# Performance work log

Hardware: AMD Instinct MI355X
Metric: run time of the kernel (lower is better)

## Reference

```python
import jax, jax.numpy as jnp
import numpy as np

N_NODES = 100000
N_EDGES = 600000
IN_SIZE = 128
OUT_SIZE = 128
N_GRAPHS = 100
BN_EPS = 1e-5


def setup_inputs() -> dict:
    key = jax.random.key(0)
    ks = jax.random.split(key, 8)
    h = jax.random.normal(ks[0], (N_NODES, IN_SIZE), dtype=jnp.float32)
    norm = jax.random.uniform(ks[1], (N_NODES, 1), dtype=jnp.float32)
    src = jax.random.randint(ks[2], (N_EDGES,), 0, N_NODES, dtype=jnp.int32)
    dst = jax.random.randint(ks[3], (N_EDGES,), 0, N_NODES, dtype=jnp.int32)
    graph_ids = jnp.sort(jax.random.randint(ks[4], (N_NODES,), 0, N_GRAPHS, dtype=jnp.int32))
    # Linear + BatchNorm params
    W = jax.random.normal(ks[5], (IN_SIZE, OUT_SIZE), dtype=jnp.float32) / np.sqrt(IN_SIZE)
    b = jnp.zeros((OUT_SIZE,), dtype=jnp.float32)
    gamma = jnp.ones((OUT_SIZE,), dtype=jnp.float32)
    beta = jnp.zeros((OUT_SIZE,), dtype=jnp.float32)
    return {"h": h, "norm": norm, "W": W, "b": b, "gamma": gamma, "beta": beta,
            "src": src, "dst": dst, "graph_ids": graph_ids}


def reference(h, norm, W, b, gamma, beta, src, dst, graph_ids):
    # pre-normalize, scatter-sum over edges (copy_src + sum), post-normalize
    x = h * norm                                            # [N, in]
    agg = jax.ops.segment_sum(x[src], dst, num_segments=N_NODES)  # SpMM
    x = agg * norm
    # linear + relu
    x = jax.nn.relu(jnp.dot(x, W) + b)                      # [N, out]
    # BatchNorm1d (training-mode: batch mean, biased variance)
    mean = jnp.mean(x, axis=0)
    var = jnp.mean(jnp.square(x - mean), axis=0)
    x = (x - mean) * jax.lax.rsqrt(var + BN_EPS) * gamma + beta
    # sum_nodes pooling per graph
    phis = jax.ops.segment_sum(x, graph_ids, num_segments=N_GRAPHS)  # [G, out]
    return (x, phis)
```

## Files before the change

### kernel.cpp

```cpp
#include <hip/hip_runtime.h>
#include <hip/hip_bf16.h>

#define N_NODES 100000
#define N_PAD 100096
#define N_EDGES 600000
#define CH 128
#define N_GRAPHS 100
#define BN_EPS 1e-5f
#define NCHUNK 391
#define NBUCKET 64
#define HIST_BLOCKS 2344
#define PRESCALE_BLOCKS 6250

typedef __bf16 bf16x8 __attribute__((ext_vector_type(8)));
typedef float f32x4 __attribute__((ext_vector_type(4)));

__device__ __forceinline__ ushort f2bf(float f) {
    union { float f; unsigned u; } x; x.f = f;
    unsigned u = x.u;
    unsigned r = (u + 0x7fffu + ((u >> 16) & 1u)) >> 16;
    return (ushort)r;
}
__device__ __forceinline__ float bflo(unsigned p) { return __builtin_bit_cast(float, p << 16); }
__device__ __forceinline__ float bfhi(unsigned p) { return __builtin_bit_cast(float, p & 0xffff0000u); }

__global__ __launch_bounds__(256) void k_front(const int* __restrict__ dst,
        const float* __restrict__ h, const float* __restrict__ norm,
        const float* __restrict__ W, int* __restrict__ cnt,
        ushort* __restrict__ xh, ushort* __restrict__ Wt) {
    unsigned bid = blockIdx.x;
    if (bid < HIST_BLOCKS) {
        int e = bid * 256 + threadIdx.x;
        if (e < N_EDGES) atomicAdd(&cnt[dst[e]], 1);
    } else if (bid < HIST_BLOCKS + PRESCALE_BLOCKS) {
        int t = (bid - HIST_BLOCKS) * 256 + threadIdx.x;
        int n = t >> 4, c = (t & 15) << 3;
        float nm = norm[n];
        float4 a = *(const float4*)(h + (size_t)n * CH + c);
        float4 d = *(const float4*)(h + (size_t)n * CH + c + 4);
        uint4 o;
        o.x = (unsigned)f2bf(a.x * nm) | ((unsigned)f2bf(a.y * nm) << 16);
        o.y = (unsigned)f2bf(a.z * nm) | ((unsigned)f2bf(a.w * nm) << 16);
        o.z = (unsigned)f2bf(d.x * nm) | ((unsigned)f2bf(d.y * nm) << 16);
        o.w = (unsigned)f2bf(d.z * nm) | ((unsigned)f2bf(d.w * nm) << 16);
        *(uint4*)(xh + (size_t)n * CH + c) = o;
    } else {
        int t = (bid - HIST_BLOCKS - PRESCALE_BLOCKS) * 256 + threadIdx.x;
        int k = t >> 7, o = t & 127;
        Wt[o * CH + k] = f2bf(W[t]);
    }
}

__global__ __launch_bounds__(256) void k_blockoffs(const int* __restrict__ cnt,
        int* __restrict__ gcursor, int* __restrict__ offs, int* __restrict__ cursor) {
    __shared__ int sm[256];
    __shared__ int base;
    int t = threadIdx.x;
    int i = blockIdx.x * 256 + t;
    int v = (i < N_NODES) ? cnt[i] : 0;
    sm[t] = v; __syncthreads();
    for (int off = 1; off < 256; off <<= 1) {
        int add = (t >= off) ? sm[t - off] : 0;
        __syncthreads();
        sm[t] += add;
        __syncthreads();
    }
    if (t == 255) base = atomicAdd(gcursor, sm[255]);
    __syncthreads();
    if (i < N_NODES) {
        int start = base + sm[t] - v;
        offs[i] = start;
        cursor[i] = start;
    }
}

__global__ __launch_bounds__(256) void k_fill(const int* __restrict__ src, const int* __restrict__ dst,
        int* __restrict__ cursor, int* __restrict__ esrc) {
    int e = blockIdx.x * 256 + threadIdx.x;
    if (e < N_EDGES) {
        int p = atomicAdd(&cursor[dst[e]], 1);
        esrc[p] = src[e];
    }
}

__global__ __launch_bounds__(256) void k_gather(const ushort* __restrict__ xh,
        const float* __restrict__ norm, const int* __restrict__ offs,
        const int* __restrict__ cnt, const int* __restrict__ esrc,
        ushort* __restrict__ x2) {
    int t = blockIdx.x * 256 + threadIdx.x;
    int n = t >> 4;
    int c = (t & 15) << 3;
    if (n >= N_PAD) return;
    int j0 = 0, e = 0;
    float nn = 0.f;
    if (n < N_NODES) { j0 = offs[n]; e = cnt[n]; nn = norm[n]; }
    float a0=0.f,a1=0.f,a2=0.f,a3=0.f,a4=0.f,a5=0.f,a6=0.f,a7=0.f;
    int j = 0;
    for (; j + 4 <= e; j += 4) {
        int s0 = esrc[j0 + j], s1 = esrc[j0 + j + 1];
        int s2 = esrc[j0 + j + 2], s3 = esrc[j0 + j + 3];
        uint4 v0 = *(const uint4*)(xh + (size_t)s0 * CH + c);
        uint4 v1 = *(const uint4*)(xh + (size_t)s1 * CH + c);
        uint4 v2 = *(const uint4*)(xh + (size_t)s2 * CH + c);
        uint4 v3 = *(const uint4*)(xh + (size_t)s3 * CH + c);
        a0 += bflo(v0.x) + bflo(v1.x) + bflo(v2.x) + bflo(v3.x);
        a1 += bfhi(v0.x) + bfhi(v1.x) + bfhi(v2.x) + bfhi(v3.x);
        a2 += bflo(v0.y) + bflo(v1.y) + bflo(v2.y) + bflo(v3.y);
        a3 += bfhi(v0.y) + bfhi(v1.y) + bfhi(v2.y) + bfhi(v3.y);
        a4 += bflo(v0.z) + bflo(v1.z) + bflo(v2.z) + bflo(v3.z);
        a5 += bfhi(v0.z) + bfhi(v1.z) + bfhi(v2.z) + bfhi(v3.z);
        a6 += bflo(v0.w) + bflo(v1.w) + bflo(v2.w) + bflo(v3.w);
        a7 += bfhi(v0.w) + bfhi(v1.w) + bfhi(v2.w) + bfhi(v3.w);
    }
    for (; j < e; j++) {
        int s = esrc[j0 + j];
        uint4 v = *(const uint4*)(xh + (size_t)s * CH + c);
        a0 += bflo(v.x); a1 += bfhi(v.x);
        a2 += bflo(v.y); a3 += bfhi(v.y);
        a4 += bflo(v.z); a5 += bfhi(v.z);
        a6 += bflo(v.w); a7 += bfhi(v.w);
    }
    uint4 o;
    o.x = (unsigned)f2bf(a0 * nn) | ((unsigned)f2bf(a1 * nn) << 16);
    o.y = (unsigned)f2bf(a2 * nn) | ((unsigned)f2bf(a3 * nn) << 16);
    o.z = (unsigned)f2bf(a4 * nn) | ((unsigned)f2bf(a5 * nn) << 16);
    o.w = (unsigned)f2bf(a6 * nn) | ((unsigned)f2bf(a7 * nn) << 16);
    *(uint4*)(x2 + (size_t)n * CH + c) = o;
}

__global__ __launch_bounds__(256) void k_gemm(const ushort* __restrict__ x2,
        const ushort* __restrict__ Wt, const float* __restrict__ bias,
        ushort* __restrict__ y16, float* __restrict__ psum, float* __restrict__ psq) {
    __shared__ ushort ys[128 * CH];

    int tid = threadIdx.x;
    int w = tid >> 6, L = tid & 63;
    int c15 = L & 15, quad = L >> 4;
    size_t nb = (size_t)blockIdx.x * 128 + w * 32;

    const bf16x8* A0 = (const bf16x8*)(x2 + (nb + c15) * CH);
    const bf16x8* A1 = (const bf16x8*)(x2 + (nb + 16 + c15) * CH);

    f32x4 acc0[8] = {}, acc1[8] = {};
    #pragma unroll
    for (int kt = 0; kt < 4; kt++) {
        bf16x8 a0 = A0[kt * 4 + quad];
        bf16x8 a1 = A1[kt * 4 + quad];
        #pragma unroll
        for (int ot = 0; ot < 8; ot++) {
            bf16x8 b = *(const bf16x8*)(Wt + (size_t)(ot * 16 + c15) * CH + kt * 32 + quad * 8);
            acc0[ot] = __builtin_amdgcn_mfma_f32_16x16x32_bf16(a0, b, acc0[ot], 0, 0, 0);
            acc1[ot] = __builtin_amdgcn_mfma_f32_16x16x32_bf16(a1, b, acc1[ot], 0, 0, 0);
        }
    }

    float sA[8], qA[8];
    #pragma unroll
    for (int ot = 0; ot < 8; ot++) {
        int col = ot * 16 + c15;
        float bv = bias[col];
        float s_ = 0.f, q_ = 0.f;
        #pragma unroll
        for (int r = 0; r < 4; r++) {
            size_t n = nb + quad * 4 + r;
            float v = fmaxf(acc0[ot][r] + bv, 0.f);
            ys[(w * 32 + quad * 4 + r) * CH + col] = f2bf(v);
            if (n < N_NODES) { s_ += v; q_ += v * v; }
            size_t n2 = n + 16;
            float v2 = fmaxf(acc1[ot][r] + bv, 0.f);
            ys[(w * 32 + 16 + quad * 4 + r) * CH + col] = f2bf(v2);
            if (n2 < N_NODES) { s_ += v2; q_ += v2 * v2; }
        }
        sA[ot] = s_; qA[ot] = q_;
    }
    __syncthreads();

    {
        const uint4* ysv = (const uint4*)ys;
        uint4* out = (uint4*)(y16 + (size_t)blockIdx.x * 128 * CH);
        #pragma unroll
        for (int i = 0; i < 8; i++) out[tid + i * 256] = ysv[tid + i * 256];
    }
    __syncthreads();

    float* red = (float*)ys;
    #pragma unroll
    for (int ot = 0; ot < 8; ot++) {
        red[ot * 256 + tid] = sA[ot];
        red[2048 + ot * 256 + tid] = qA[ot];
    }
    __syncthreads();

    if (tid < 128) {
        int ot = tid >> 4, cc = tid & 15;
        int col = ot * 16 + cc;
        float S = 0.f, Q = 0.f;
        #pragma unroll
        for (int g = 0; g < 16; g++) {
            int sl = (g >> 2) * 64 + (g & 3) * 16 + cc;
            S += red[ot * 256 + sl];
            Q += red[2048 + ot * 256 + sl];
        }
        int bucket = blockIdx.x & (NBUCKET - 1);
        atomicAdd(&psum[bucket * CH + col], S);
        atomicAdd(&psq[bucket * CH + col], Q);
    }
}

__global__ void k_finalize(const float* __restrict__ psum, const float* __restrict__ psq,
        const float* __restrict__ gamma, const float* __restrict__ beta,
        float* __restrict__ scale, float* __restrict__ shift, float* __restrict__ phis) {
    int t = threadIdx.x;
    float S = 0.f, Q = 0.f;
    for (int g = 0; g < NBUCKET; g++) { S += psum[g * CH + t]; Q += psq[g * CH + t]; }
    const float invN = 1.f / (float)N_NODES;
    float mean = S * invN;
    float var  = Q * invN - mean * mean;
    float sc   = gamma[t] * rsqrtf(var + BN_EPS);
    scale[t] = sc;
    shift[t] = beta[t] - mean * sc;
    for (int i = t; i < N_GRAPHS * CH; i += 128) phis[i] = 0.f;
}

__global__ __launch_bounds__(256) void k_bnpool(const ushort* __restrict__ y16,
        const int* __restrict__ gids, const float* __restrict__ scale,
        const float* __restrict__ shift, float* __restrict__ xout,
        float* __restrict__ phis) {
    __shared__ float smP[16][CH];

    int tid = threadIdx.x;
    int cg = tid & 15, rl = tid >> 4;
    int c = cg * 8;
    int r0 = blockIdx.x * 256;
    int rbase = r0 + rl * 16;

    float4 sc0 = *(const float4*)(scale + c), sc1 = *(const float4*)(scale + c + 4);
    float4 sh0 = *(const float4*)(shift + c), sh1 = *(const float4*)(shift + c + 4);

    bool fast = (r0 + 255 < N_NODES) && (gids[r0] == gids[r0 + 255]);

    if (fast) {
        float4 p0 = make_float4(0.f,0.f,0.f,0.f), p1 = make_float4(0.f,0.f,0.f,0.f);
        for (int j = 0; j < 16; j++) {
            int r = rbase + j;
            uint4 v = *(const uint4*)(y16 + (size_t)r * CH + c);
            float4 f0, f1;
            f0.x = fmaf(bflo(v.x), sc0.x, sh0.x); f0.y = fmaf(bfhi(v.x), sc0.y, sh0.y);
            f0.z = fmaf(bflo(v.y), sc0.z, sh0.z); f0.w = fmaf(bfhi(v.y), sc0.w, sh0.w);
            f1.x = fmaf(bflo(v.z), sc1.x, sh1.x); f1.y = fmaf(bfhi(v.z), sc1.y, sh1.y);
            f1.z = fmaf(bflo(v.w), sc1.z, sh1.z); f1.w = fmaf(bfhi(v.w), sc1.w, sh1.w);
            *(float4*)(xout + (size_t)r * CH + c) = f0;
            *(float4*)(xout + (size_t)r * CH + c + 4) = f1;
            p0.x += f0.x; p0.y += f0.y; p0.z += f0.z; p0.w += f0.w;
            p1.x += f1.x; p1.y += f1.y; p1.z += f1.z; p1.w += f1.w;
        }
        *(float4*)&smP[rl][c] = p0;
        *(float4*)&smP[rl][c + 4] = p1;
        __syncthreads();
        if (tid < 128) {
            int g = gids[r0];
            float S = 0.f;
            #pragma unroll
            for (int k = 0; k < 16; k++) S += smP[k][tid];
            atomicAdd(&phis[(size_t)g * CH + tid], S);
        }
    } else {
        float p[8] = {};
        int gprev = -1;
        for (int j = 0; j < 16; j++) {
            int r = rbase + j;
            if (r >= N_NODES) break;
            int g = gids[r];
            if (g != gprev) {
                if (gprev >= 0) {
                    #pragma unroll
                    for (int k = 0; k < 8; k++) {
                        atomicAdd(&phis[(size_t)gprev * CH + c + k], p[k]);
                        p[k] = 0.f;
                    }
                }
                gprev = g;
            }
            uint4 v = *(const uint4*)(y16 + (size_t)r * CH + c);
            float f[8];
            f[0] = fmaf(bflo(v.x), sc0.x, sh0.x); f[1] = fmaf(bfhi(v.x), sc0.y, sh0.y);
            f[2] = fmaf(bflo(v.y), sc0.z, sh0.z); f[3] = fmaf(bfhi(v.y), sc0.w, sh0.w);
            f[4] = fmaf(bflo(v.z), sc1.x, sh1.x); f[5] = fmaf(bfhi(v.z), sc1.y, sh1.y);
            f[6] = fmaf(bflo(v.w), sc1.z, sh1.z); f[7] = fmaf(bfhi(v.w), sc1.w, sh1.w);
            *(float4*)(xout + (size_t)r * CH + c) = make_float4(f[0], f[1], f[2], f[3]);
            *(float4*)(xout + (size_t)r * CH + c + 4) = make_float4(f[4], f[5], f[6], f[7]);
            #pragma unroll
            for (int k = 0; k < 8; k++) p[k] += f[k];
        }
        if (gprev >= 0) {
            #pragma unroll
            for (int k = 0; k < 8; k++)
                atomicAdd(&phis[(size_t)gprev * CH + c + k], p[k]);
        }
    }
}

extern "C" void kernel_launch(void* const* d_in, const int* in_sizes, int n_in,
                              void* d_out, int out_size, void* d_ws, size_t ws_size,
                              hipStream_t stream)
{
    const float* h     = (const float*)d_in[0];
    const float* norm  = (const float*)d_in[1];
    const float* W     = (const float*)d_in[2];
    const float* b     = (const float*)d_in[3];
    const float* gamma = (const float*)d_in[4];
    const float* beta  = (const float*)d_in[5];
    const int*   src   = (const int*)d_in[6];
    const int*   dst   = (const int*)d_in[7];
    const int*   gids  = (const int*)d_in[8];

    float* x_out = (float*)d_out;
    float* phis  = x_out + (size_t)N_NODES * CH;

    ushort* xh   = (ushort*)d_ws;
    ushort* x2   = xh + (size_t)N_NODES * CH;
    ushort* y16  = x2 + (size_t)N_PAD * CH;
    ushort* Wt   = y16 + (size_t)N_PAD * CH;
    int*   cnt     = (int*)(Wt + CH * CH);
    int*   gcursor = cnt + N_NODES;
    float* psum    = (float*)(gcursor + 1);
    float* psq     = psum + NBUCKET * CH;
    int*   offs    = (int*)(psq + NBUCKET * CH);
    int*   cursor  = offs + N_NODES;
    int*   esrc    = cursor + N_NODES;
    float* scale   = (float*)(esrc + N_EDGES);
    float* shift   = scale + CH;

    hipMemsetAsync(cnt, 0, (size_t)(N_NODES + 1 + 2 * NBUCKET * CH) * sizeof(int), stream);

    k_front<<<HIST_BLOCKS + PRESCALE_BLOCKS + 64, 256, 0, stream>>>(dst, h, norm, W, cnt, xh, Wt);
    k_blockoffs<<<NCHUNK, 256, 0, stream>>>(cnt, gcursor, offs, cursor);
    k_fill<<<(N_EDGES + 255) / 256, 256, 0, stream>>>(src, dst, cursor, esrc);
    k_gather<<<N_PAD / 16, 256, 0, stream>>>(xh, norm, offs, cnt, esrc, x2);
    k_gemm<<<N_PAD / 128, 256, 0, stream>>>(x2, Wt, b, y16, psum, psq);
    k_finalize<<<1, 128, 0, stream>>>(psum, psq, gamma, beta, scale, shift, phis);
    k_bnpool<<<(N_NODES + 255) / 256, 256, 0, stream>>>(y16, gids, scale, shift, x_out, phis);
}
```

Baseline: 258.5 us.

## Replace CSR build with fixed-capacity per-node edge buckets plus overflow list

Drops the histogram, prefix-scan and fill kernels. Edges are now bucketed in one pass inside the front kernel, where an atomic counter per destination node assigns each edge a slot in a fixed 32-slot bucket, and extra edges go to a global overflow list that the gather kernel scans linearly. This removes two kernel launches and a second atomic pass over the edges. The cost is a larger, sparser esrc array (100k×32 ints) and a sequential overflow scan that every thread must run if any node has more than 32 in-edges. Edges beyond 8192 overflow entries would be silently dropped.

```diff
diff --git a/kernel.cpp b/kernel.cpp
--- a/kernel.cpp
+++ b/kernel.cpp
@@ -7,9 +7,10 @@
 #define CH 128
 #define N_GRAPHS 100
 #define BN_EPS 1e-5f
-#define NCHUNK 391
 #define NBUCKET 64
-#define HIST_BLOCKS 2344
+#define CAP 32
+#define OVFCAP 8192
+#define FILL_BLOCKS 586
 #define PRESCALE_BLOCKS 6250
 
 typedef __bf16 bf16x8 __attribute__((ext_vector_type(8)));
@@ -24,16 +25,32 @@
 __device__ __forceinline__ float bflo(unsigned p) { return __builtin_bit_cast(float, p << 16); }
 __device__ __forceinline__ float bfhi(unsigned p) { return __builtin_bit_cast(float, p & 0xffff0000u); }
 
-__global__ __launch_bounds__(256) void k_front(const int* __restrict__ dst,
-        const float* __restrict__ h, const float* __restrict__ norm,
-        const float* __restrict__ W, int* __restrict__ cnt,
-        ushort* __restrict__ xh, ushort* __restrict__ Wt) {
+__global__ __launch_bounds__(256) void k_front(const int* __restrict__ src,
+        const int* __restrict__ dst, const float* __restrict__ h,
+        const float* __restrict__ norm, const float* __restrict__ W,
+        int* __restrict__ cnt, int* __restrict__ ovfcur, int* __restrict__ ovf,
+        int* __restrict__ esrc, ushort* __restrict__ xh, ushort* __restrict__ Wt) {
     unsigned bid = blockIdx.x;
-    if (bid < HIST_BLOCKS) {
-        int e = bid * 256 + threadIdx.x;
-        if (e < N_EDGES) atomicAdd(&cnt[dst[e]], 1);
-    } else if (bid < HIST_BLOCKS + PRESCALE_BLOCKS) {
-        int t = (bid - HIST_BLOCKS) * 256 + threadIdx.x;
+    if (bid < FILL_BLOCKS) {
+        int e0 = (bid * 256 + threadIdx.x) * 4;
+        if (e0 < N_EDGES) {
+            int4 d = *(const int4*)(dst + e0);
+            int4 s = *(const int4*)(src + e0);
+            int s0 = atomicAdd(&cnt[d.x], 1);
+            int s1 = atomicAdd(&cnt[d.y], 1);
+            int s2 = atomicAdd(&cnt[d.z], 1);
+            int s3 = atomicAdd(&cnt[d.w], 1);
+            if (s0 < CAP) esrc[d.x * CAP + s0] = s.x;
+            else { int p = atomicAdd(ovfcur, 1); if (p < OVFCAP) { ovf[2*p] = d.x; ovf[2*p+1] = s.x; } }
+            if (s1 < CAP) esrc[d.y * CAP + s1] = s.y;
+            else { int p = atomicAdd(ovfcur, 1); if (p < OVFCAP) { ovf[2*p] = d.y; ovf[2*p+1] = s.y; } }
+            if (s2 < CAP) esrc[d.z * CAP + s2] = s.z;
+            else { int p = atomicAdd(ovfcur, 1); if (p < OVFCAP) { ovf[2*p] = d.z; ovf[2*p+1] = s.z; } }
+            if (s3 < CAP) esrc[d.w * CAP + s3] = s.w;
+            else { int p = atomicAdd(ovfcur, 1); if (p < OVFCAP) { ovf[2*p] = d.w; ovf[2*p+1] = s.w; } }
+        }
+    } else if (bid < FILL_BLOCKS + PRESCALE_BLOCKS) {
+        int t = (bid - FILL_BLOCKS) * 256 + threadIdx.x;
         int n = t >> 4, c = (t & 15) << 3;
         float nm = norm[n];
         float4 a = *(const float4*)(h + (size_t)n * CH + c);
@@ -45,60 +62,29 @@
         o.w = (unsigned)f2bf(d.z * nm) | ((unsigned)f2bf(d.w * nm) << 16);
         *(uint4*)(xh + (size_t)n * CH + c) = o;
     } else {
-        int t = (bid - HIST_BLOCKS - PRESCALE_BLOCKS) * 256 + threadIdx.x;
+        int t = (bid - FILL_BLOCKS - PRESCALE_BLOCKS) * 256 + threadIdx.x;
         int k = t >> 7, o = t & 127;
         Wt[o * CH + k] = f2bf(W[t]);
     }
 }
 
-__global__ __launch_bounds__(256) void k_blockoffs(const int* __restrict__ cnt,
-        int* __restrict__ gcursor, int* __restrict__ offs, int* __restrict__ cursor) {
-    __shared__ int sm[256];
-    __shared__ int base;
-    int t = threadIdx.x;
-    int i = blockIdx.x * 256 + t;
-    int v = (i < N_NODES) ? cnt[i] : 0;
-    sm[t] = v; __syncthreads();
-    for (int off = 1; off < 256; off <<= 1) {
-        int add = (t >= off) ? sm[t - off] : 0;
-        __syncthreads();
-        sm[t] += add;
-        __syncthreads();
-    }
-    if (t == 255) base = atomicAdd(gcursor, sm[255]);
-    __syncthreads();
-    if (i < N_NODES) {
-        int start = base + sm[t] - v;
-        offs[i] = start;
-        cursor[i] = start;
-    }
-}
-
-__global__ __launch_bounds__(256) void k_fill(const int* __restrict__ src, const int* __restrict__ dst,
-        int* __restrict__ cursor, int* __restrict__ esrc) {
-    int e = blockIdx.x * 256 + threadIdx.x;
-    if (e < N_EDGES) {
-        int p = atomicAdd(&cursor[dst[e]], 1);
-        esrc[p] = src[e];
-    }
-}
-
 __global__ __launch_bounds__(256) void k_gather(const ushort* __restrict__ xh,
-        const float* __restrict__ norm, const int* __restrict__ offs,
-        const int* __restrict__ cnt, const int* __restrict__ esrc,
-        ushort* __restrict__ x2) {
+        const float* __restrict__ norm, const int* __restrict__ cnt,
+        const int* __restrict__ esrc, const int* __restrict__ ovfcur,
+        const int* __restrict__ ovf, ushort* __restrict__ x2) {
     int t = blockIdx.x * 256 + threadIdx.x;
     int n = t >> 4;
     int c = (t & 15) << 3;
     if (n >= N_PAD) return;
-    int j0 = 0, e = 0;
+    int e = 0;
     float nn = 0.f;
-    if (n < N_NODES) { j0 = offs[n]; e = cnt[n]; nn = norm[n]; }
+    if (n < N_NODES) { e = min(cnt[n], CAP); nn = norm[n]; }
+    int base = n * CAP;
     float a0=0.f,a1=0.f,a2=0.f,a3=0.f,a4=0.f,a5=0.f,a6=0.f,a7=0.f;
     int j = 0;
     for (; j + 4 <= e; j += 4) {
-        int s0 = esrc[j0 + j], s1 = esrc[j0 + j + 1];
-        int s2 = esrc[j0 + j + 2], s3 = esrc[j0 + j + 3];
+        int s0 = esrc[base + j], s1 = esrc[base + j + 1];
+        int s2 = esrc[base + j + 2], s3 = esrc[base + j + 3];
         uint4 v0 = *(const uint4*)(xh + (size_t)s0 * CH + c);
         uint4 v1 = *(const uint4*)(xh + (size_t)s1 * CH + c);
         uint4 v2 = *(const uint4*)(xh + (size_t)s2 * CH + c);
@@ -113,12 +99,28 @@
         a7 += bfhi(v0.w) + bfhi(v1.w) + bfhi(v2.w) + bfhi(v3.w);
     }
     for (; j < e; j++) {
-        int s = esrc[j0 + j];
+        int s = esrc[base + j];
         uint4 v = *(const uint4*)(xh + (size_t)s * CH + c);
         a0 += bflo(v.x); a1 += bfhi(v.x);
         a2 += bflo(v.y); a3 += bfhi(v.y);
         a4 += bflo(v.z); a5 += bfhi(v.z);
         a6 += bflo(v.w); a7 += bfhi(v.w);
+    }
+    if (n < N_NODES) {
+        int no = *ovfcur;
+        if (no > 0) {
+            no = min(no, OVFCAP);
+            for (int i = 0; i < no; i++) {
+                if (ovf[2*i] == n) {
+                    int s = ovf[2*i+1];
+                    uint4 v = *(const uint4*)(xh + (size_t)s * CH + c);
+                    a0 += bflo(v.x); a1 += bfhi(v.x);
+                    a2 += bflo(v.y); a3 += bfhi(v.y);
+                    a4 += bflo(v.z); a5 += bfhi(v.z);
+                    a6 += bflo(v.w); a7 += bfhi(v.w);
+                }
+            }
+        }
     }
     uint4 o;
     o.x = (unsigned)f2bf(a0 * nn) | ((unsigned)f2bf(a1 * nn) << 16);
@@ -322,21 +324,19 @@
     ushort* y16  = x2 + (size_t)N_PAD * CH;
     ushort* Wt   = y16 + (size_t)N_PAD * CH;
     int*   cnt     = (int*)(Wt + CH * CH);
-    int*   gcursor = cnt + N_NODES;
-    float* psum    = (float*)(gcursor + 1);
+    float* psum    = (float*)(cnt + N_NODES);
     float* psq     = psum + NBUCKET * CH;
-    int*   offs    = (int*)(psq + NBUCKET * CH);
-    int*   cursor  = offs + N_NODES;
-    int*   esrc    = cursor + N_NODES;
-    float* scale   = (float*)(esrc + N_EDGES);
+    int*   ovfcur  = (int*)(psq + NBUCKET * CH);
+    int*   esrc    = ovfcur + 4;
+    int*   ovf     = esrc + (size_t)N_NODES * CAP;
+    float* scale   = (float*)(ovf + 2 * OVFCAP);
     float* shift   = scale + CH;
 
-    hipMemsetAsync(cnt, 0, (size_t)(N_NODES + 1 + 2 * NBUCKET * CH) * sizeof(int), stream);
-
-    k_front<<<HIST_BLOCKS + PRESCALE_BLOCKS + 64, 256, 0, stream>>>(dst, h, norm, W, cnt, xh, Wt);
-    k_blockoffs<<<NCHUNK, 256, 0, stream>>>(cnt, gcursor, offs, cursor);
-    k_fill<<<(N_EDGES + 255) / 256, 256, 0, stream>>>(src, dst, cursor, esrc);
-    k_gather<<<N_PAD / 16, 256, 0, stream>>>(xh, norm, offs, cnt, esrc, x2);
+    hipMemsetAsync(cnt, 0, (size_t)(N_NODES + 2 * NBUCKET * CH + 4) * sizeof(int), stream);
+
+    k_front<<<FILL_BLOCKS + PRESCALE_BLOCKS + 64, 256, 0, stream>>>(
+        src, dst, h, norm, W, cnt, ovfcur, ovf, esrc, xh, Wt);
+    k_gather<<<N_PAD / 16, 256, 0, stream>>>(xh, norm, cnt, esrc, ovfcur, ovf, x2);
     k_gemm<<<N_PAD / 128, 256, 0, stream>>>(x2, Wt, b, y16, psum, psq);
     k_finalize<<<1, 128, 0, stream>>>(psum, psq, gamma, beta, scale, shift, phis);
     k_bnpool<<<(N_NODES + 255) / 256, 256, 0, stream>>>(y16, gids, scale, shift, x_out, phis);
```

After: 229.2 us. 11.3% less time.
